# Kernel tuning notes

Hardware: AMD Instinct MI355X
Metric: run time of the kernel (lower is better)

The kernel has to match this reference:

```python
import jax, jax.numpy as jnp
import numpy as np

L, N, E, NODE_D, EDGE_D, H = 3, 50000, 800000, 64, 16, 128
EPS = 1e-5


def _ln(x, g, b):
    mu = jnp.mean(x, axis=-1, keepdims=True)
    var = jnp.var(x, axis=-1, keepdims=True)
    return (x - mu) * jax.lax.rsqrt(var + EPS) * g + b


def setup_inputs() -> dict:
    key = jax.random.key(0)
    ks = jax.random.split(key, 16)
    inp = {
        "x": jax.random.normal(ks[0], (N, NODE_D), dtype=jnp.float32),
        "edge_index": jax.random.randint(ks[1], (2, E), 0, N, dtype=jnp.int64 if jax.config.jax_enable_x64 else jnp.int32),
        "edge_attr": jax.random.normal(ks[2], (E, EDGE_D), dtype=jnp.float32),
        # node_embed: Linear(node_dim, H) + LayerNorm
        "node_W": jax.random.normal(ks[3], (H, NODE_D), dtype=jnp.float32) * (2.0 / H) ** 0.5,
        "node_b": jnp.zeros((H,), jnp.float32),
        "node_ln_g": jnp.ones((H,), jnp.float32),
        "node_ln_b": jnp.zeros((H,), jnp.float32),
        # per-layer GINConv params, stacked on leading layer dim
        "edge_W": jax.random.normal(ks[4], (L, H, EDGE_D), dtype=jnp.float32) * (2.0 / H) ** 0.5,
        "edge_b": jnp.zeros((L, H), jnp.float32),
        "edge_ln_g": jnp.ones((L, H), jnp.float32),
        "edge_ln_b": jnp.zeros((L, H), jnp.float32),
        "sl_attr": jax.random.normal(ks[5], (L, 1, EDGE_D), dtype=jnp.float32),
        "mlp_W1": jax.random.normal(ks[6], (L, 2 * H, H), dtype=jnp.float32) * (1.0 / H) ** 0.5,
        "mlp_b1": jnp.zeros((L, 2 * H), jnp.float32),
        "mlp_W2": jax.random.normal(ks[7], (L, H, 2 * H), dtype=jnp.float32) * (1.0 / (2 * H)) ** 0.5,
        "mlp_b2": jnp.zeros((L, H), jnp.float32),
        # BatchNorm1d affine params (batch-stat / training-mode math)
        "bn_g": jnp.ones((L, H), jnp.float32),
        "bn_b": jnp.zeros((L, H), jnp.float32),
    }
    return inp


def reference(x, edge_index, edge_attr, node_W, node_b, node_ln_g, node_ln_b,
              edge_W, edge_b, edge_ln_g, edge_ln_b, sl_attr,
              mlp_W1, mlp_b1, mlp_W2, mlp_b2, bn_g, bn_b):
    n = x.shape[0]
    # augmented edge list with self loops appended (add_self_loops)
    loop = jnp.arange(n, dtype=edge_index.dtype)
    src = jnp.concatenate([edge_index[0], loop])  # [E+N]
    dst = jnp.concatenate([edge_index[1], loop])  # [E+N]

    # node_embed: Linear -> LN -> ReLU
    h = jax.nn.relu(_ln(x @ node_W.T + node_b, node_ln_g, node_ln_b))

    for l in range(L):
        # edge_embed on [original edges ; learned self-loop attr]
        sl = jnp.broadcast_to(sl_attr[l], (n, EDGE_D))
        ea = jnp.concatenate([edge_attr, sl], axis=0)          # [E+N, edge_dim]
        ea = jax.nn.relu(_ln(ea @ edge_W[l].T + edge_b[l], edge_ln_g[l], edge_ln_b[l]))
        # message: gather x_j + edge_attr; aggregate: scatter-add to dst
        msg = h[src] + ea                                      # [E+N, H]
        aggr = jax.ops.segment_sum(msg, dst, num_segments=n)   # [N, H]
        # update MLP: Linear -> GELU -> Linear (dropout inactive at eval)
        z = jax.nn.gelu(aggr @ mlp_W1[l].T + mlp_b1[l], approximate=False)
        hl = z @ mlp_W2[l].T + mlp_b2[l]
        # BatchNorm1d (training-mode batch statistics over node dim)
        mu = jnp.mean(hl, axis=0, keepdims=True)
        var = jnp.var(hl, axis=0, keepdims=True)
        hl = (hl - mu) * jax.lax.rsqrt(var + EPS) * bn_g[l] + bn_b[l]
        if l != L - 1:
            hl = jax.nn.relu(hl)  # drop_ratio = 0 -> dropout is identity
        h = hl
    return h
```

## Files before the change

### kernel.cpp

```cpp
#include <hip/hip_runtime.h>
#include <cstdint>
#include <cstddef>

#define HD 128
#define EDGED 16
#define NODED 64
#define LN_EPS 1e-5f

typedef __bf16 bf16x8 __attribute__((ext_vector_type(8)));
typedef float  f32x4  __attribute__((ext_vector_type(4)));
typedef _Float16 half2v __attribute__((ext_vector_type(2)));
typedef _Float16 half4v __attribute__((ext_vector_type(4)));
typedef _Float16 half8v __attribute__((ext_vector_type(8)));

union HU { half8v v; half2v p[4]; };

__device__ __forceinline__ float gelu_exact(float x) {
    return 0.5f * x * (1.0f + erff(x * 0.7071067811865475f));
}

__device__ __forceinline__ float hi16_to_f(int bits) {
    union { unsigned short u; _Float16 h; } c;
    c.u = (unsigned short)((unsigned)bits >> 16);
    return (float)c.h;
}

__global__ void wconv_k(const float* __restrict__ in, __bf16* __restrict__ hi,
                        __bf16* __restrict__ lo, int n) {
    int i = blockIdx.x * blockDim.x + threadIdx.x;
    if (i < n) {
        float v = in[i];
        __bf16 h = (__bf16)v;
        hi[i] = h;
        lo[i] = (__bf16)(v - (float)h);
    }
}

__global__ void wconv16_k(const float* __restrict__ in, _Float16* __restrict__ hi,
                          _Float16* __restrict__ lo, int n) {
    int i = blockIdx.x * blockDim.x + threadIdx.x;
    if (i < n) {
        float v = in[i];
        _Float16 h = (_Float16)v;
        hi[i] = h;
        lo[i] = (_Float16)(v - (float)h);
    }
}


__global__ void hist_k(const int* __restrict__ ei, int* __restrict__ cnt, int E) {
    int e = blockIdx.x * blockDim.x + threadIdx.x;
    if (e < E) atomicAdd(&cnt[ei[E + e]], 1);
}

__global__ void scan1_k(const int* __restrict__ in, int* __restrict__ out,
                        int* __restrict__ bsum, int n) {
    __shared__ int lds[256];
    int t = threadIdx.x;
    int i = blockIdx.x * 256 + t;
    int v = (i < n) ? in[i] : 0;
    lds[t] = v;
    __syncthreads();
#pragma unroll
    for (int o = 1; o < 256; o <<= 1) {
        int u = (t >= o) ? lds[t - o] : 0;
        __syncthreads();
        lds[t] += u;
        __syncthreads();
    }
    if (i < n) out[i] = lds[t] - v;
    if (t == 255) bsum[blockIdx.x] = lds[255];
}

__global__ void scan2_k(const int* __restrict__ bsum, int* __restrict__ boff, int nb) {
    __shared__ int lds[256];
    int t = threadIdx.x;
    int v = (t < nb) ? bsum[t] : 0;
    lds[t] = v;
    __syncthreads();
#pragma unroll
    for (int o = 1; o < 256; o <<= 1) {
        int u = (t >= o) ? lds[t - o] : 0;
        __syncthreads();
        lds[t] += u;
        __syncthreads();
    }
    if (t < nb) boff[t] = lds[t] - v;
}

__global__ void scan3_k(int* __restrict__ rs, int* __restrict__ cursor,
                        const int* __restrict__ boff, int n, int E) {
    int i = blockIdx.x * 256 + threadIdx.x;
    if (i < n) {
        int v = rs[i] + boff[blockIdx.x];
        rs[i] = v;
        cursor[i] = v;
    }
    if (i == 0) rs[n] = E;
}

__global__ void scatter_k(const int* __restrict__ ei, int* __restrict__ cursor,
                          int2* __restrict__ es, int E) {
    int e = blockIdx.x * blockDim.x + threadIdx.x;
    if (e < E) {
        int dst = ei[E + e];
        int slot = atomicAdd(&cursor[dst], 1);
        es[slot] = make_int2(ei[e], e);
    }
}

__global__ void prep_k(const float* __restrict__ edge_W, const float* __restrict__ edge_b,
                       const float* __restrict__ edge_g, const float* __restrict__ edge_be,
                       const float* __restrict__ sl_attr, _Float16* __restrict__ Wg16_3,
                       float* __restrict__ bg3, float* __restrict__ M3,
                       float* __restrict__ v3, float* __restrict__ s03,
                       float* __restrict__ slv3)
{
    const int l = blockIdx.x;
    const float* W = edge_W + (size_t)l * HD * EDGED;
    const float* b = edge_b + l * HD;
    const float* g = edge_g + l * HD;
    __shared__ float Wp[HD * EDGED];
    __shared__ float bp[HD];
    __shared__ float wm[EDGED];
    __shared__ float Msh[256];
    __shared__ float vsh[EDGED];
    __shared__ float ash[EDGED];
    __shared__ float bmS, s0sh;
    const int t = threadIdx.x;
#pragma unroll
    for (int m = 0; m < 8; ++m) Wp[m * 256 + t] = W[m * 256 + t];
    __syncthreads();
    if (t < EDGED) {
        float s = 0.f;
        for (int c = 0; c < HD; ++c) s += Wp[c * EDGED + t];
        wm[t] = s * (1.f / HD);
    } else if (t == EDGED) {
        float s = 0.f;
        for (int c = 0; c < HD; ++c) s += b[c];
        bmS = s * (1.f / HD);
    }
    __syncthreads();
    if (t < HD) bp[t] = b[t] - bmS;
    __syncthreads();
#pragma unroll
    for (int m = 0; m < 8; ++m) {
        int idx = m * 256 + t;
        int c = idx >> 4, k = idx & 15;
        float val = Wp[idx] - wm[k];
        Wp[idx] = val;
        Wg16_3[(size_t)l * 2048 + idx] = (_Float16)(val * g[c]);
    }
    if (t < HD) bg3[l * HD + t] = bp[t] * g[t];
    __syncthreads();
    {
        int k = t >> 4, j = t & 15;
        float s = 0.f;
        for (int c = 0; c < HD; ++c) s += Wp[c * EDGED + k] * Wp[c * EDGED + j];
        Msh[t] = s;
        M3[l * 256 + t] = s;
    }
    if (t < EDGED) {
        float s = 0.f;
        for (int c = 0; c < HD; ++c) s += Wp[c * EDGED + t] * bp[c];
        vsh[t] = 2.f * s;
        v3[l * EDGED + t] = 2.f * s;
        ash[t] = sl_attr[l * EDGED + t];
    } else if (t == EDGED) {
        float s = 0.f;
        for (int c = 0; c < HD; ++c) s += bp[c] * bp[c];
        s0sh = s;
        s03[l] = s;
    }
    __syncthreads();
    if (t < HD) {
        float q = s0sh;
#pragma unroll
        for (int k = 0; k < EDGED; ++k) {
            float tk = vsh[k];
#pragma unroll
            for (int j = 0; j < EDGED; ++j) tk = fmaf(Msh[k * 16 + j], ash[j], tk);
            q = fmaf(ash[k], tk, q);
        }
        float inv = rsqrtf(q * (1.f / HD) + LN_EPS);
        float y = 0.f;
#pragma unroll
        for (int k = 0; k < EDGED; ++k) y = fmaf(Wp[t * EDGED + k], ash[k], y);
        slv3[l * HD + t] = fmaxf(fmaf(fmaf(y, g[t], bg3[l * HD + t]), inv, edge_be[l * HD + t]), 0.f);
    }
}

__launch_bounds__(256)
__global__ void einv_k(const int2* __restrict__ es, const float* __restrict__ eattr,
                       const float* __restrict__ M3, const float* __restrict__ v3,
                       const float* __restrict__ s03, unsigned* __restrict__ sei,
                       _Float16* __restrict__ attr16, int E)
{
    __shared__ float Ms[3 * 256];
    __shared__ float vs[3 * 16];
    __shared__ float s0s[4];
    const int t = threadIdx.x;
    for (int i = t; i < 768; i += 256) Ms[i] = M3[i];
    if (t < 48) vs[t] = v3[t];
    if (t < 3) s0s[t] = s03[t];
    __syncthreads();
    int slot = blockIdx.x * 256 + t;
    if (slot >= E) return;
    int2 se = es[slot];
    const float4* ap = (const float4*)(eattr + (size_t)se.y * EDGED);
    float4 A0 = ap[0], A1 = ap[1], A2 = ap[2], A3 = ap[3];
    float a[16] = {A0.x, A0.y, A0.z, A0.w, A1.x, A1.y, A1.z, A1.w,
                   A2.x, A2.y, A2.z, A2.w, A3.x, A3.y, A3.z, A3.w};
    {
        half8v o0, o1;
#pragma unroll
        for (int i = 0; i < 8; ++i) { o0[i] = (_Float16)a[i]; o1[i] = (_Float16)a[8 + i]; }
        _Float16* op = attr16 + (size_t)slot * EDGED;
        *(half8v*)&op[0] = o0;
        *(half8v*)&op[8] = o1;
    }
#pragma unroll
    for (int l = 0; l < 3; ++l) {
        float q = s0s[l];
#pragma unroll
        for (int k = 0; k < 16; ++k) {
            const float* Mr = &Ms[l * 256 + k * 16];
            float tk = vs[l * 16 + k];
#pragma unroll
            for (int j = 0; j < 16; ++j) tk = fmaf(Mr[j], a[j], tk);
            q = fmaf(a[k], tk, q);
        }
        float iv = rsqrtf(q * (1.f / HD) + LN_EPS);
        union { _Float16 h; unsigned short u; } cv;
        cv.h = (_Float16)iv;
        sei[(size_t)l * E + slot] = ((unsigned)se.x & 0xFFFFu) | ((unsigned)cv.u << 16);
    }
}

template<int K, int NC, int ACT, int STATS, int AMODE, int OUTMODE>
__launch_bounds__(256)
__global__ void mgemm_k(const void* __restrict__ Ap1, const void* __restrict__ Ap2,
                        const void* __restrict__ Wp1, const void* __restrict__ Wp2,
                        const float* __restrict__ bias, float* __restrict__ C,
                        void* __restrict__ Co1, int M, float* __restrict__ stats)
{
    constexpr int RG = 2;
    constexpr int NT = 4;
    constexpr int NK = K / 32;
    __shared__ float st_lds[2][64];

    const int t    = threadIdx.x;
    const int lane = t & 63;
    const int wv   = t >> 6;
    const int ln15 = lane & 15;
    const int quad = lane >> 4;
    const int row_base = blockIdx.x * 128 + wv * 32;
    const int col0 = blockIdx.y * 64;

    f32x4 acc[RG][NT];
#pragma unroll
    for (int g = 0; g < RG; ++g)
#pragma unroll
        for (int nt = 0; nt < NT; ++nt)
#pragma unroll
            for (int r = 0; r < 4; ++r) acc[g][nt][r] = 0.f;

    size_t arow[RG];
#pragma unroll
    for (int g = 0; g < RG; ++g) {
        int row = row_base + g * 16 + ln15;
        row = row < M ? row : M - 1;
        arow[g] = (size_t)row * K + quad * 8;
    }
    size_t brow[NT];
#pragma unroll
    for (int nt = 0; nt < NT; ++nt)
        brow[nt] = (size_t)(col0 + nt * 16 + ln15) * K + quad * 8;

    if constexpr (AMODE == 0) {
        const __bf16* Ahi = (const __bf16*)Ap1;
        const __bf16* Alo = (const __bf16*)Ap2;
        const __bf16* Whi = (const __bf16*)Wp1;
        const __bf16* Wlo = (const __bf16*)Wp2;
        bf16x8 a0h[RG], a0l[RG], a1h[RG], a1l[RG];
        bf16x8 b0h[NT], b0l[NT], b1h[NT], b1l[NT];

#define LD_A(kc, AH, AL) { \
    _Pragma("unroll") \
    for (int g = 0; g < RG; ++g) { \
        AH[g] = *(const bf16x8*)(Ahi + arow[g] + (kc)); \
        AL[g] = *(const bf16x8*)(Alo + arow[g] + (kc)); \
    } }
#define LD_B(kc, BH, BL) { \
    _Pragma("unroll") \
    for (int nt = 0; nt < NT; ++nt) { \
        BH[nt] = *(const bf16x8*)(Whi + brow[nt] + (kc)); \
        BL[nt] = *(const bf16x8*)(Wlo + brow[nt] + (kc)); \
    } }
#define DO_MFMA(AH, AL, BH, BL) { \
    _Pragma("unroll") \
    for (int nt = 0; nt < NT; ++nt) { \
        _Pragma("unroll") \
        for (int g = 0; g < RG; ++g) { \
            acc[g][nt] = __builtin_amdgcn_mfma_f32_16x16x32_bf16(AH[g], BH[nt], acc[g][nt], 0, 0, 0); \
            acc[g][nt] = __builtin_amdgcn_mfma_f32_16x16x32_bf16(AH[g], BL[nt], acc[g][nt], 0, 0, 0); \
            acc[g][nt] = __builtin_amdgcn_mfma_f32_16x16x32_bf16(AL[g], BH[nt], acc[g][nt], 0, 0, 0); \
        } } }

        LD_A(0, a0h, a0l);
        LD_B(0, b0h, b0l);
        for (int s = 0; s < NK; s += 2) {
            LD_A((s + 1) * 32, a1h, a1l);
            LD_B((s + 1) * 32, b1h, b1l);
            DO_MFMA(a0h, a0l, b0h, b0l);
            if (s + 2 < NK) {
                LD_A((s + 2) * 32, a0h, a0l);
                LD_B((s + 2) * 32, b0h, b0l);
            }
            DO_MFMA(a1h, a1l, b1h, b1l);
        }
#undef LD_A
#undef LD_B
#undef DO_MFMA
    } else {
        const _Float16* Af = (const _Float16*)Ap1;
        const _Float16* Wh = (const _Float16*)Wp1;
        const _Float16* Wl = (const _Float16*)Wp2;
        half8v a0[RG], a1[RG];
        half8v b0h[NT], b0l[NT], b1h[NT], b1l[NT];

#define LD_A16(kc, A) { \
    _Pragma("unroll") \
    for (int g = 0; g < RG; ++g) A[g] = *(const half8v*)(Af + arow[g] + (kc)); }
#define LD_B16(kc, BH, BL) { \
    _Pragma("unroll") \
    for (int nt = 0; nt < NT; ++nt) { \
        BH[nt] = *(const half8v*)(Wh + brow[nt] + (kc)); \
        BL[nt] = *(const half8v*)(Wl + brow[nt] + (kc)); \
    } }
#define DO_MFMA16(A, BH, BL) { \
    _Pragma("unroll") \
    for (int nt = 0; nt < NT; ++nt) { \
        _Pragma("unroll") \
        for (int g = 0; g < RG; ++g) { \
            acc[g][nt] = __builtin_amdgcn_mfma_f32_16x16x32_f16(A[g], BH[nt], acc[g][nt], 0, 0, 0); \
            acc[g][nt] = __builtin_amdgcn_mfma_f32_16x16x32_f16(A[g], BL[nt], acc[g][nt], 0, 0, 0); \
        } } }

        LD_A16(0, a0);
        LD_B16(0, b0h, b0l);
        for (int s = 0; s < NK; s += 2) {
            LD_A16((s + 1) * 32, a1);
            LD_B16((s + 1) * 32, b1h, b1l);
            DO_MFMA16(a0, b0h, b0l);
            if (s + 2 < NK) {
                LD_A16((s + 2) * 32, a0);
                LD_B16((s + 2) * 32, b0h, b0l);
            }
            DO_MFMA16(a1, b1h, b1l);
        }
#undef LD_A16
#undef LD_B16
#undef DO_MFMA16
    }

    if (STATS) {
        if (t < 64) { st_lds[0][t] = 0.f; st_lds[1][t] = 0.f; }
        __syncthreads();
    }

    float bv[NT];
#pragma unroll
    for (int nt = 0; nt < NT; ++nt) bv[nt] = bias[col0 + nt * 16 + ln15];

    float s1[NT], s2[NT];
#pragma unroll
    for (int nt = 0; nt < NT; ++nt) { s1[nt] = 0.f; s2[nt] = 0.f; }

#pragma unroll
    for (int g = 0; g < RG; ++g)
#pragma unroll
        for (int r = 0; r < 4; ++r) {
            int row = row_base + g * 16 + quad * 4 + r;
            if (row < M) {
#pragma unroll
                for (int nt = 0; nt < NT; ++nt) {
                    float v = acc[g][nt][r] + bv[nt];
                    if (ACT == 1) v = gelu_exact(v);
                    size_t ci = (size_t)row * NC + col0 + nt * 16 + ln15;
                    if (OUTMODE == 2) {
                        ((_Float16*)Co1)[ci] = (_Float16)v;
                    } else {
                        C[ci] = v;
                    }
                    if (STATS) { s1[nt] += v; s2[nt] += v * v; }
                }
            }
        }

    if (STATS) {
#pragma unroll
        for (int nt = 0; nt < NT; ++nt) {
            atomicAdd(&st_lds[0][nt * 16 + ln15], s1[nt]);
            atomicAdd(&st_lds[1][nt * 16 + ln15], s2[nt]);
        }
        __syncthreads();
        if (t < 64) {
            atomicAdd(&stats[col0 + t],      st_lds[0][t]);
            atomicAdd(&stats[HD + col0 + t], st_lds[1][t]);
        }
    }
}

__launch_bounds__(256)
__global__ void nemb_k(const __bf16* __restrict__ Ahi, const __bf16* __restrict__ Alo,
                       const __bf16* __restrict__ Whi, const __bf16* __restrict__ Wlo,
                       const float* __restrict__ bias, const float* __restrict__ gam,
                       const float* __restrict__ bet, _Float16* __restrict__ h16, int M)
{
    constexpr int RG = 2;
    constexpr int NT = 8;
    const int t    = threadIdx.x;
    const int lane = t & 63;
    const int wv   = t >> 6;
    const int ln15 = lane & 15;
    const int quad = lane >> 4;
    const int row_base = blockIdx.x * 128 + wv * 32;

    f32x4 acc[RG][NT];
#pragma unroll
    for (int g = 0; g < RG; ++g)
#pragma unroll
        for (int nt = 0; nt < NT; ++nt)
#pragma unroll
            for (int r = 0; r < 4; ++r) acc[g][nt][r] = 0.f;

    size_t arow[RG];
#pragma unroll
    for (int g = 0; g < RG; ++g) {
        int row = row_base + g * 16 + ln15;
        row = row < M ? row : M - 1;
        arow[g] = (size_t)row * NODED + quad * 8;
    }
    size_t brow[NT];
#pragma unroll
    for (int nt = 0; nt < NT; ++nt)
        brow[nt] = (size_t)(nt * 16 + ln15) * NODED + quad * 8;

#pragma unroll
    for (int s = 0; s < 2; ++s) {
        bf16x8 ah[RG], al[RG];
#pragma unroll
        for (int g = 0; g < RG; ++g) {
            ah[g] = *(const bf16x8*)(Ahi + arow[g] + s * 32);
            al[g] = *(const bf16x8*)(Alo + arow[g] + s * 32);
        }
#pragma unroll
        for (int nt = 0; nt < NT; ++nt) {
            bf16x8 bh = *(const bf16x8*)(Whi + brow[nt] + s * 32);
            bf16x8 bl = *(const bf16x8*)(Wlo + brow[nt] + s * 32);
#pragma unroll
            for (int g = 0; g < RG; ++g) {
                acc[g][nt] = __builtin_amdgcn_mfma_f32_16x16x32_bf16(ah[g], bh, acc[g][nt], 0, 0, 0);
                acc[g][nt] = __builtin_amdgcn_mfma_f32_16x16x32_bf16(ah[g], bl, acc[g][nt], 0, 0, 0);
                acc[g][nt] = __builtin_amdgcn_mfma_f32_16x16x32_bf16(al[g], bh, acc[g][nt], 0, 0, 0);
            }
        }
    }

    float bv[NT], gv[NT], betv[NT];
#pragma unroll
    for (int nt = 0; nt < NT; ++nt) {
        int col = nt * 16 + ln15;
        bv[nt]   = bias[col];
        gv[nt]   = gam[col];
        betv[nt] = bet[col];
    }

#pragma unroll
    for (int g = 0; g < RG; ++g)
#pragma unroll
        for (int r = 0; r < 4; ++r) {
            int row = row_base + g * 16 + quad * 4 + r;
            float v[NT];
            float s = 0.f, q = 0.f;
#pragma unroll
            for (int nt = 0; nt < NT; ++nt) {
                v[nt] = acc[g][nt][r] + bv[nt];
                s += v[nt];
                q += v[nt] * v[nt];
            }
#pragma unroll
            for (int o = 8; o > 0; o >>= 1) {
                s += __shfl_xor(s, o, 64);
                q += __shfl_xor(q, o, 64);
            }
            float mu  = s * (1.f / 128.f);
            float inv = rsqrtf(q * (1.f / 128.f) - mu * mu + LN_EPS);
            if (row < M) {
#pragma unroll
                for (int nt = 0; nt < NT; ++nt) {
                    float rr = fmaxf(fmaf((v[nt] - mu) * inv, gv[nt], betv[nt]), 0.f);
                    h16[(size_t)row * HD + nt * 16 + ln15] = (_Float16)rr;
                }
            }
        }
}

__launch_bounds__(256)
__global__ void pull9_k(const _Float16* __restrict__ h16, const int* __restrict__ rs,
                        const _Float16* __restrict__ attr16, const unsigned* __restrict__ sei,
                        const float* __restrict__ slv, const _Float16* __restrict__ Wg16,
                        const float* __restrict__ bg, const float* __restrict__ bet,
                        __bf16* __restrict__ Ahi, __bf16* __restrict__ Alo, int N)
{
    __shared__ _Float16 alds_all[4][64 * EDGED];
    const int t = threadIdx.x;
    const int lane = t & 63;
    const int wv = t >> 6;
    _Float16* alds = alds_all[wv];
    uint4* alds4 = (uint4*)alds;

    const int c0 = lane * 2;
    half2v w0p[8], w1p[8];
#pragma unroll
    for (int k = 0; k < 8; ++k) {
        w0p[k] = *(const half2v*)&Wg16[c0 * EDGED + 2 * k];
        w1p[k] = *(const half2v*)&Wg16[(c0 + 1) * EDGED + 2 * k];
    }
    const float2 bgv  = *(const float2*)&bg[c0];
    const float2 btv  = *(const float2*)&bet[c0];
    const float2 slvv = *(const float2*)&slv[c0];

    const int stride = gridDim.x << 2;
    for (int n = (blockIdx.x << 2) + wv; n < N; n += stride) {
        half2v hs = *(const half2v*)&h16[(size_t)n * HD + c0];
        float acc0 = (float)hs.x + slvv.x;
        float acc1 = (float)hs.y + slvv.y;

        const int beg = rs[n], end = rs[n + 1];
        for (int s0 = beg; s0 < end; s0 += 64) {
            int m = end - s0; if (m > 64) m = 64;
            int sv = 0;
            if (lane < m) sv = (int)sei[s0 + lane];
            const uint4* src4 = (const uint4*)(attr16 + (size_t)s0 * EDGED);
#pragma unroll
            for (int it = 0; it < 2; ++it) {
                int idx = (it << 6) + lane;
                if (idx < (m << 1)) alds4[idx] = src4[idx];
            }
            asm volatile("s_waitcnt lgkmcnt(0)" ::: "memory");

#define EDGE_BODY(JJ, IVJ, HVJ) { \
            HU ua, ub; \
            ua.v = *(const half8v*)&alds[(JJ) * EDGED]; \
            ub.v = *(const half8v*)&alds[(JJ) * EDGED + 8]; \
            float p0 = bgv.x, q0 = 0.f, p1 = bgv.y, q1 = 0.f; \
            p0 = __builtin_amdgcn_fdot2(ua.p[0], w0p[0], p0, false); \
            q0 = __builtin_amdgcn_fdot2(ua.p[1], w0p[1], q0, false); \
            p1 = __builtin_amdgcn_fdot2(ua.p[0], w1p[0], p1, false); \
            q1 = __builtin_amdgcn_fdot2(ua.p[1], w1p[1], q1, false); \
            p0 = __builtin_amdgcn_fdot2(ua.p[2], w0p[2], p0, false); \
            q0 = __builtin_amdgcn_fdot2(ua.p[3], w0p[3], q0, false); \
            p1 = __builtin_amdgcn_fdot2(ua.p[2], w1p[2], p1, false); \
            q1 = __builtin_amdgcn_fdot2(ua.p[3], w1p[3], q1, false); \
            p0 = __builtin_amdgcn_fdot2(ub.p[0], w0p[4], p0, false); \
            q0 = __builtin_amdgcn_fdot2(ub.p[1], w0p[5], q0, false); \
            p1 = __builtin_amdgcn_fdot2(ub.p[0], w1p[4], p1, false); \
            q1 = __builtin_amdgcn_fdot2(ub.p[1], w1p[5], q1, false); \
            p0 = __builtin_amdgcn_fdot2(ub.p[2], w0p[6], p0, false); \
            q0 = __builtin_amdgcn_fdot2(ub.p[3], w0p[7], q0, false); \
            p1 = __builtin_amdgcn_fdot2(ub.p[2], w1p[6], p1, false); \
            q1 = __builtin_amdgcn_fdot2(ub.p[3], w1p[7], q1, false); \
            acc0 += fmaxf(fmaf(p0 + q0, IVJ, btv.x), 0.f) + (float)HVJ.x; \
            acc1 += fmaxf(fmaf(p1 + q1, IVJ, btv.y), 0.f) + (float)HVJ.y; \
        }

            int j = 0;
            for (; j + 4 <= m; j += 4) {
                int v0 = __shfl(sv, j,     64);
                int v1 = __shfl(sv, j + 1, 64);
                int v2 = __shfl(sv, j + 2, 64);
                int v3 = __shfl(sv, j + 3, 64);
                int s_0 = v0 & 0xFFFF, s_1 = v1 & 0xFFFF;
                int s_2 = v2 & 0xFFFF, s_3 = v3 & 0xFFFF;
                float i0 = hi16_to_f(v0);
                float i1 = hi16_to_f(v1);
                float i2 = hi16_to_f(v2);
                float i3 = hi16_to_f(v3);
                half2v h0 = *(const half2v*)&h16[(size_t)s_0 * HD + c0];
                half2v h1 = *(const half2v*)&h16[(size_t)s_1 * HD + c0];
                half2v h2 = *(const half2v*)&h16[(size_t)s_2 * HD + c0];
                half2v h3 = *(const half2v*)&h16[(size_t)s_3 * HD + c0];
                EDGE_BODY(j,     i0, h0);
                EDGE_BODY(j + 1, i1, h1);
                EDGE_BODY(j + 2, i2, h2);
                EDGE_BODY(j + 3, i3, h3);
            }
            for (; j < m; ++j) {
                int vj = __shfl(sv, j, 64);
                int s_ = vj & 0xFFFF;
                float ij = hi16_to_f(vj);
                half2v hj = *(const half2v*)&h16[(size_t)s_ * HD + c0];
                EDGE_BODY(j, ij, hj);
            }
#undef EDGE_BODY
        }
        __bf16 b0 = (__bf16)acc0, b1 = (__bf16)acc1;
        union { __bf16 b[2]; unsigned u; } ph, pl;
        ph.b[0] = b0;
        ph.b[1] = b1;
        pl.b[0] = (__bf16)(acc0 - (float)b0);
        pl.b[1] = (__bf16)(acc1 - (float)b1);
        *(unsigned*)&Ahi[(size_t)n * HD + c0] = ph.u;
        *(unsigned*)&Alo[(size_t)n * HD + c0] = pl.u;
    }
}

__global__ void bn_k(const _Float16* __restrict__ hl, const float* __restrict__ stats,
                     const float* __restrict__ gam, const float* __restrict__ bet,
                     float* __restrict__ out32, _Float16* __restrict__ out16,
                     int total4, float invN, int relu)
{
    int idx = blockIdx.x * blockDim.x + threadIdx.x;
    if (idx < total4) {
        int c4 = idx & 31;
        half4v xh = *(const half4v*)&hl[(size_t)idx * 4];
        float4 s1 = ((const float4*)stats)[c4];
        float4 s2 = ((const float4*)stats)[32 + c4];
        float4 g  = ((const float4*)gam)[c4];
        float4 b  = ((const float4*)bet)[c4];
        float4 r;
        {
            float m = s1.x * invN; float v = s2.x * invN - m * m;
            r.x = fmaf(((float)xh.x - m) * rsqrtf(v + LN_EPS), g.x, b.x);
        }
        {
            float m = s1.y * invN; float v = s2.y * invN - m * m;
            r.y = fmaf(((float)xh.y - m) * rsqrtf(v + LN_EPS), g.y, b.y);
        }
        {
            float m = s1.z * invN; float v = s2.z * invN - m * m;
            r.z = fmaf(((float)xh.z - m) * rsqrtf(v + LN_EPS), g.z, b.z);
        }
        {
            float m = s1.w * invN; float v = s2.w * invN - m * m;
            r.w = fmaf(((float)xh.w - m) * rsqrtf(v + LN_EPS), g.w, b.w);
        }
        if (relu) {
            r.x = fmaxf(r.x, 0.f); r.y = fmaxf(r.y, 0.f);
            r.z = fmaxf(r.z, 0.f); r.w = fmaxf(r.w, 0.f);
        }
        if (out16) {
            half4v o;
            o.x = (_Float16)r.x; o.y = (_Float16)r.y;
            o.z = (_Float16)r.z; o.w = (_Float16)r.w;
            *(half4v*)&out16[(size_t)idx * 4] = o;
        } else {
            ((float4*)out32)[idx] = r;
        }
    }
}

extern "C" void kernel_launch(void* const* d_in, const int* in_sizes, int n_in,
                              void* d_out, int out_size, void* d_ws, size_t ws_size,
                              hipStream_t stream)
{
    const float* x       = (const float*)d_in[0];
    const int*   ei      = (const int*)d_in[1];
    const float* eattr   = (const float*)d_in[2];
    const float* node_W  = (const float*)d_in[3];
    const float* node_b  = (const float*)d_in[4];
    const float* node_g  = (const float*)d_in[5];
    const float* node_be = (const float*)d_in[6];
    const float* edge_W  = (const float*)d_in[7];
    const float* edge_b  = (const float*)d_in[8];
    const float* edge_g  = (const float*)d_in[9];
    const float* edge_be = (const float*)d_in[10];
    const float* sl_attr = (const float*)d_in[11];
    const float* W1      = (const float*)d_in[12];
    const float* b1      = (const float*)d_in[13];
    const float* W2      = (const float*)d_in[14];
    const float* b2      = (const float*)d_in[15];
    const float* bn_g    = (const float*)d_in[16];
    const float* bn_b    = (const float*)d_in[17];

    const int N = in_sizes[0] / NODED;
    const int E = in_sizes[1] / 2;

    char* base = (char*)d_ws;
    size_t off = 0;
    auto take = [&](size_t nbytes) -> void* {
        void* p = base + off;
        off = (off + nbytes + 15) & ~(size_t)15;
        return p;
    };
    _Float16* h16  = (_Float16*)take((size_t)N * HD * 2);
    _Float16* hl16 = (_Float16*)take((size_t)N * HD * 2);
    __bf16* aghi   = (__bf16*)take((size_t)N * HD * 2);
    __bf16* aglo   = (__bf16*)take((size_t)N * HD * 2);
    _Float16* z16  = (_Float16*)take((size_t)N * 256 * 2);
    __bf16* xhi    = (__bf16*)take((size_t)N * NODED * 2);
    __bf16* xlo    = (__bf16*)take((size_t)N * NODED * 2);
    float*  slv3   = (float*)take(3 * HD * 4);
    float*  stats  = (float*)take(3 * 256 * 4);
    int*    cnt    = (int*)take((size_t)N * 4);
    int*    cursor = (int*)take((size_t)N * 4);
    int*    bsum   = (int*)take(256 * 4);
    int*    boff   = (int*)take(256 * 4);
    int*    rs     = (int*)take(((size_t)N + 2) * 4);
    int2*   es     = (int2*)take((size_t)E * 8);
    unsigned* sei  = (unsigned*)take((size_t)3 * E * 4);
    _Float16* attr16 = (_Float16*)take((size_t)E * EDGED * 2);
    _Float16* Wg16_3 = (_Float16*)take(3 * 2048 * 2);
    float*  bg3    = (float*)take(3 * HD * 4);
    float*  M3     = (float*)take(3 * 256 * 4);
    float*  v3     = (float*)take(3 * 16 * 4);
    float*  s03    = (float*)take(4 * 4);
    __bf16* nWhi   = (__bf16*)take((size_t)HD * NODED * 2);
    __bf16* nWlo   = (__bf16*)take((size_t)HD * NODED * 2);
    __bf16* W1hi   = (__bf16*)take((size_t)3 * 256 * HD * 2);
    __bf16* W1lo   = (__bf16*)take((size_t)3 * 256 * HD * 2);
    _Float16* W2h16 = (_Float16*)take((size_t)3 * HD * 256 * 2);
    _Float16* W2l16 = (_Float16*)take((size_t)3 * HD * 256 * 2);

    wconv_k<<<(HD * NODED + 255) / 256, 256, 0, stream>>>(node_W, nWhi, nWlo, HD * NODED);
    wconv_k<<<(3 * 256 * HD + 255) / 256, 256, 0, stream>>>(W1, W1hi, W1lo, 3 * 256 * HD);
    wconv16_k<<<(3 * 256 * HD + 255) / 256, 256, 0, stream>>>(W2, W2h16, W2l16, 3 * 256 * HD);
    wconv_k<<<((int)((size_t)N * NODED + 255) / 256), 256, 0, stream>>>(x, xhi, xlo, N * NODED);

    prep_k<<<3, 256, 0, stream>>>(edge_W, edge_b, edge_g, edge_be, sl_attr,
                                  Wg16_3, bg3, M3, v3, s03, slv3);

    const int eblocks = (E + 255) / 256;
    const int nblocks = (N + 255) / 256;
    hipMemsetAsync(cnt, 0, (size_t)N * sizeof(int), stream);
    hist_k<<<eblocks, 256, 0, stream>>>(ei, cnt, E);
    scan1_k<<<nblocks, 256, 0, stream>>>(cnt, rs, bsum, N);
    scan2_k<<<1, 256, 0, stream>>>(bsum, boff, nblocks);
    scan3_k<<<nblocks, 256, 0, stream>>>(rs, cursor, boff, N, E);
    scatter_k<<<eblocks, 256, 0, stream>>>(ei, cursor, es, E);

    einv_k<<<eblocks, 256, 0, stream>>>(es, eattr, M3, v3, s03, sei, attr16, E);

    const int total4  = N * (HD / 4);
    const int vblocks = (total4 + 255) / 256;
    const int gb128   = (N + 127) / 128;
    int pgrid = (N + 3) / 4;
    if (pgrid > 2048) pgrid = 2048;

    nemb_k<<<gb128, 256, 0, stream>>>(xhi, xlo, nWhi, nWlo, node_b,
                                      node_g, node_be, h16, N);

    hipMemsetAsync(stats, 0, 3 * 256 * sizeof(float), stream);

    for (int l = 0; l < 3; ++l) {
        pull9_k<<<pgrid, 256, 0, stream>>>(h16, rs, attr16, sei + (size_t)l * E,
                                           slv3 + l * HD, Wg16_3 + (size_t)l * 2048,
                                           bg3 + l * HD, edge_be + l * HD,
                                           aghi, aglo, N);

        mgemm_k<HD, 256, 1, 0, 0, 2><<<dim3(gb128, 4), 256, 0, stream>>>(
            aghi, aglo, W1hi + (size_t)l * 256 * HD, W1lo + (size_t)l * 256 * HD,
            b1 + l * 256, nullptr, z16, N, nullptr);

        mgemm_k<256, HD, 0, 1, 1, 2><<<dim3(gb128, 2), 256, 0, stream>>>(
            z16, nullptr, W2h16 + (size_t)l * HD * 256, W2l16 + (size_t)l * HD * 256,
            b2 + l * HD, nullptr, hl16, N, stats + l * 256);

        bn_k<<<vblocks, 256, 0, stream>>>(hl16, stats + l * 256,
                                          bn_g + l * HD, bn_b + l * HD,
                                          (float*)d_out, (l < 2) ? h16 : nullptr,
                                          total4, 1.f / N, (l < 2) ? 1 : 0);
    }
}
```

Measured before the change: 871.7 us.

## Fuse the two MLP GEMMs into one kernel keeping GELU activations in LDS

Replaces the two separate MLP GEMM launches with a single kernel. Each wave computes its 32x256 GELU intermediate into shared memory, then runs the second GEMM from LDS and accumulates the BatchNorm statistics. This removes the global write and re-read of the N x 256 half-precision intermediate and one launch per layer. In exchange it uses 64KB of LDS per block, which limits occupancy, and the software double-buffering of the first GEMM's loads is dropped.

```diff
diff --git a/kernel.cpp b/kernel.cpp
--- a/kernel.cpp
+++ b/kernel.cpp
@@ -237,17 +237,17 @@
     }
 }
 
-template<int K, int NC, int ACT, int STATS, int AMODE, int OUTMODE>
 __launch_bounds__(256)
-__global__ void mgemm_k(const void* __restrict__ Ap1, const void* __restrict__ Ap2,
-                        const void* __restrict__ Wp1, const void* __restrict__ Wp2,
-                        const float* __restrict__ bias, float* __restrict__ C,
-                        void* __restrict__ Co1, int M, float* __restrict__ stats)
+__global__ void fmlp_k(const __bf16* __restrict__ Ahi, const __bf16* __restrict__ Alo,
+                       const __bf16* __restrict__ W1hi, const __bf16* __restrict__ W1lo,
+                       const float* __restrict__ b1, const _Float16* __restrict__ W2h,
+                       const _Float16* __restrict__ W2l, const float* __restrict__ b2,
+                       _Float16* __restrict__ hl16, int M, float* __restrict__ stats)
 {
     constexpr int RG = 2;
-    constexpr int NT = 4;
-    constexpr int NK = K / 32;
-    __shared__ float st_lds[2][64];
+    constexpr int NT = 8;
+    __shared__ _Float16 zlds_all[4][32 * 256];
+    __shared__ float st_lds[2][128];
 
     const int t    = threadIdx.x;
     const int lane = t & 63;
@@ -255,127 +255,99 @@
     const int ln15 = lane & 15;
     const int quad = lane >> 4;
     const int row_base = blockIdx.x * 128 + wv * 32;
-    const int col0 = blockIdx.y * 64;
-
-    f32x4 acc[RG][NT];
-#pragma unroll
-    for (int g = 0; g < RG; ++g)
-#pragma unroll
-        for (int nt = 0; nt < NT; ++nt)
-#pragma unroll
-            for (int r = 0; r < 4; ++r) acc[g][nt][r] = 0.f;
+    _Float16* zl = zlds_all[wv];
 
     size_t arow[RG];
 #pragma unroll
     for (int g = 0; g < RG; ++g) {
         int row = row_base + g * 16 + ln15;
         row = row < M ? row : M - 1;
-        arow[g] = (size_t)row * K + quad * 8;
-    }
-    size_t brow[NT];
-#pragma unroll
-    for (int nt = 0; nt < NT; ++nt)
-        brow[nt] = (size_t)(col0 + nt * 16 + ln15) * K + quad * 8;
-
-    if constexpr (AMODE == 0) {
-        const __bf16* Ahi = (const __bf16*)Ap1;
-        const __bf16* Alo = (const __bf16*)Ap2;
-        const __bf16* Whi = (const __bf16*)Wp1;
-        const __bf16* Wlo = (const __bf16*)Wp2;
-        bf16x8 a0h[RG], a0l[RG], a1h[RG], a1l[RG];
-        bf16x8 b0h[NT], b0l[NT], b1h[NT], b1l[NT];
-
-#define LD_A(kc, AH, AL) { \
-    _Pragma("unroll") \
-    for (int g = 0; g < RG; ++g) { \
-        AH[g] = *(const bf16x8*)(Ahi + arow[g] + (kc)); \
-        AL[g] = *(const bf16x8*)(Alo + arow[g] + (kc)); \
-    } }
-#define LD_B(kc, BH, BL) { \
-    _Pragma("unroll") \
-    for (int nt = 0; nt < NT; ++nt) { \
-        BH[nt] = *(const bf16x8*)(Whi + brow[nt] + (kc)); \
-        BL[nt] = *(const bf16x8*)(Wlo + brow[nt] + (kc)); \
-    } }
-#define DO_MFMA(AH, AL, BH, BL) { \
-    _Pragma("unroll") \
-    for (int nt = 0; nt < NT; ++nt) { \
-        _Pragma("unroll") \
-        for (int g = 0; g < RG; ++g) { \
-            acc[g][nt] = __builtin_amdgcn_mfma_f32_16x16x32_bf16(AH[g], BH[nt], acc[g][nt], 0, 0, 0); \
-            acc[g][nt] = __builtin_amdgcn_mfma_f32_16x16x32_bf16(AH[g], BL[nt], acc[g][nt], 0, 0, 0); \
-            acc[g][nt] = __builtin_amdgcn_mfma_f32_16x16x32_bf16(AL[g], BH[nt], acc[g][nt], 0, 0, 0); \
-        } } }
-
-        LD_A(0, a0h, a0l);
-        LD_B(0, b0h, b0l);
-        for (int s = 0; s < NK; s += 2) {
-            LD_A((s + 1) * 32, a1h, a1l);
-            LD_B((s + 1) * 32, b1h, b1l);
-            DO_MFMA(a0h, a0l, b0h, b0l);
-            if (s + 2 < NK) {
-                LD_A((s + 2) * 32, a0h, a0l);
-                LD_B((s + 2) * 32, b0h, b0l);
-            }
-            DO_MFMA(a1h, a1l, b1h, b1l);
-        }
-#undef LD_A
-#undef LD_B
-#undef DO_MFMA
-    } else {
-        const _Float16* Af = (const _Float16*)Ap1;
-        const _Float16* Wh = (const _Float16*)Wp1;
-        const _Float16* Wl = (const _Float16*)Wp2;
-        half8v a0[RG], a1[RG];
-        half8v b0h[NT], b0l[NT], b1h[NT], b1l[NT];
-
-#define LD_A16(kc, A) { \
-    _Pragma("unroll") \
-    for (int g = 0; g < RG; ++g) A[g] = *(const half8v*)(Af + arow[g] + (kc)); }
-#define LD_B16(kc, BH, BL) { \
-    _Pragma("unroll") \
-    for (int nt = 0; nt < NT; ++nt) { \
-        BH[nt] = *(const half8v*)(Wh + brow[nt] + (kc)); \
-        BL[nt] = *(const half8v*)(Wl + brow[nt] + (kc)); \
-    } }
-#define DO_MFMA16(A, BH, BL) { \
-    _Pragma("unroll") \
-    for (int nt = 0; nt < NT; ++nt) { \
-        _Pragma("unroll") \
-        for (int g = 0; g < RG; ++g) { \
-            acc[g][nt] = __builtin_amdgcn_mfma_f32_16x16x32_f16(A[g], BH[nt], acc[g][nt], 0, 0, 0); \
-            acc[g][nt] = __builtin_amdgcn_mfma_f32_16x16x32_f16(A[g], BL[nt], acc[g][nt], 0, 0, 0); \
-        } } }
-
-        LD_A16(0, a0);
-        LD_B16(0, b0h, b0l);
-        for (int s = 0; s < NK; s += 2) {
-            LD_A16((s + 1) * 32, a1);
-            LD_B16((s + 1) * 32, b1h, b1l);
-            DO_MFMA16(a0, b0h, b0l);
-            if (s + 2 < NK) {
-                LD_A16((s + 2) * 32, a0);
-                LD_B16((s + 2) * 32, b0h, b0l);
-            }
-            DO_MFMA16(a1, b1h, b1l);
-        }
-#undef LD_A16
-#undef LD_B16
-#undef DO_MFMA16
-    }
-
-    if (STATS) {
-        if (t < 64) { st_lds[0][t] = 0.f; st_lds[1][t] = 0.f; }
-        __syncthreads();
-    }
-
-    float bv[NT];
-#pragma unroll
-    for (int nt = 0; nt < NT; ++nt) bv[nt] = bias[col0 + nt * 16 + ln15];
-
-    float s1[NT], s2[NT];
-#pragma unroll
-    for (int nt = 0; nt < NT; ++nt) { s1[nt] = 0.f; s2[nt] = 0.f; }
+        arow[g] = (size_t)row * HD + quad * 8;
+    }
+
+#pragma unroll
+    for (int h = 0; h < 2; ++h) {
+        const int col0 = h * 128;
+        f32x4 acc[RG][NT];
+#pragma unroll
+        for (int g = 0; g < RG; ++g)
+#pragma unroll
+            for (int nt = 0; nt < NT; ++nt)
+#pragma unroll
+                for (int r = 0; r < 4; ++r) acc[g][nt][r] = 0.f;
+
+#pragma unroll
+        for (int s = 0; s < 4; ++s) {
+            bf16x8 ah[RG], al[RG];
+#pragma unroll
+            for (int g = 0; g < RG; ++g) {
+                ah[g] = *(const bf16x8*)(Ahi + arow[g] + s * 32);
+                al[g] = *(const bf16x8*)(Alo + arow[g] + s * 32);
+            }
+#pragma unroll
+            for (int nt = 0; nt < NT; ++nt) {
+                size_t br = (size_t)(col0 + nt * 16 + ln15) * HD + quad * 8 + s * 32;
+                bf16x8 bh = *(const bf16x8*)(W1hi + br);
+                bf16x8 bl = *(const bf16x8*)(W1lo + br);
+#pragma unroll
+                for (int g = 0; g < RG; ++g) {
+                    acc[g][nt] = __builtin_amdgcn_mfma_f32_16x16x32_bf16(ah[g], bh, acc[g][nt], 0, 0, 0);
+                    acc[g][nt] = __builtin_amdgcn_mfma_f32_16x16x32_bf16(ah[g], bl, acc[g][nt], 0, 0, 0);
+                    acc[g][nt] = __builtin_amdgcn_mfma_f32_16x16x32_bf16(al[g], bh, acc[g][nt], 0, 0, 0);
+                }
+            }
+        }
+
+#pragma unroll
+        for (int g = 0; g < RG; ++g)
+#pragma unroll
+            for (int r = 0; r < 4; ++r) {
+                int lr = g * 16 + quad * 4 + r;
+#pragma unroll
+                for (int nt = 0; nt < NT; ++nt) {
+                    int col = col0 + nt * 16 + ln15;
+                    float v = gelu_exact(acc[g][nt][r] + b1[col]);
+                    zl[lr * 256 + col] = (_Float16)v;
+                }
+            }
+    }
+
+    if (t < 128) { st_lds[0][t] = 0.f; st_lds[1][t] = 0.f; }
+    __syncthreads();
+
+    f32x4 acc2[RG][NT];
+#pragma unroll
+    for (int g = 0; g < RG; ++g)
+#pragma unroll
+        for (int nt = 0; nt < NT; ++nt)
+#pragma unroll
+            for (int r = 0; r < 4; ++r) acc2[g][nt][r] = 0.f;
+
+#pragma unroll
+    for (int s = 0; s < 8; ++s) {
+        half8v az[RG];
+#pragma unroll
+        for (int g = 0; g < RG; ++g)
+            az[g] = *(const half8v*)&zl[(g * 16 + ln15) * 256 + s * 32 + quad * 8];
+#pragma unroll
+        for (int nt = 0; nt < NT; ++nt) {
+            size_t br = (size_t)(nt * 16 + ln15) * 256 + quad * 8 + s * 32;
+            half8v wh = *(const half8v*)(W2h + br);
+            half8v wl = *(const half8v*)(W2l + br);
+#pragma unroll
+            for (int g = 0; g < RG; ++g) {
+                acc2[g][nt] = __builtin_amdgcn_mfma_f32_16x16x32_f16(az[g], wh, acc2[g][nt], 0, 0, 0);
+                acc2[g][nt] = __builtin_amdgcn_mfma_f32_16x16x32_f16(az[g], wl, acc2[g][nt], 0, 0, 0);
+            }
+        }
+    }
+
+    float bv[NT], s1[NT], s2[NT];
+#pragma unroll
+    for (int nt = 0; nt < NT; ++nt) {
+        bv[nt] = b2[nt * 16 + ln15];
+        s1[nt] = 0.f; s2[nt] = 0.f;
+    }
 
 #pragma unroll
     for (int g = 0; g < RG; ++g)
@@ -385,30 +357,23 @@
             if (row < M) {
 #pragma unroll
                 for (int nt = 0; nt < NT; ++nt) {
-                    float v = acc[g][nt][r] + bv[nt];
-                    if (ACT == 1) v = gelu_exact(v);
-                    size_t ci = (size_t)row * NC + col0 + nt * 16 + ln15;
-                    if (OUTMODE == 2) {
-                        ((_Float16*)Co1)[ci] = (_Float16)v;
-                    } else {
-                        C[ci] = v;
-                    }
-                    if (STATS) { s1[nt] += v; s2[nt] += v * v; }
+                    float v = acc2[g][nt][r] + bv[nt];
+                    hl16[(size_t)row * HD + nt * 16 + ln15] = (_Float16)v;
+                    s1[nt] += v;
+                    s2[nt] += v * v;
                 }
             }
         }
 
-    if (STATS) {
-#pragma unroll
-        for (int nt = 0; nt < NT; ++nt) {
-            atomicAdd(&st_lds[0][nt * 16 + ln15], s1[nt]);
-            atomicAdd(&st_lds[1][nt * 16 + ln15], s2[nt]);
-        }
-        __syncthreads();
-        if (t < 64) {
-            atomicAdd(&stats[col0 + t],      st_lds[0][t]);
-            atomicAdd(&stats[HD + col0 + t], st_lds[1][t]);
-        }
+#pragma unroll
+    for (int nt = 0; nt < NT; ++nt) {
+        atomicAdd(&st_lds[0][nt * 16 + ln15], s1[nt]);
+        atomicAdd(&st_lds[1][nt * 16 + ln15], s2[nt]);
+    }
+    __syncthreads();
+    if (t < 128) {
+        atomicAdd(&stats[t],      st_lds[0][t]);
+        atomicAdd(&stats[HD + t], st_lds[1][t]);
     }
 }
 
@@ -699,7 +664,6 @@
     _Float16* hl16 = (_Float16*)take((size_t)N * HD * 2);
     __bf16* aghi   = (__bf16*)take((size_t)N * HD * 2);
     __bf16* aglo   = (__bf16*)take((size_t)N * HD * 2);
-    _Float16* z16  = (_Float16*)take((size_t)N * 256 * 2);
     __bf16* xhi    = (__bf16*)take((size_t)N * NODED * 2);
     __bf16* xlo    = (__bf16*)take((size_t)N * NODED * 2);
     float*  slv3   = (float*)take(3 * HD * 4);
@@ -760,13 +724,10 @@
                                            bg3 + l * HD, edge_be + l * HD,
                                            aghi, aglo, N);
 
-        mgemm_k<HD, 256, 1, 0, 0, 2><<<dim3(gb128, 4), 256, 0, stream>>>(
+        fmlp_k<<<gb128, 256, 0, stream>>>(
             aghi, aglo, W1hi + (size_t)l * 256 * HD, W1lo + (size_t)l * 256 * HD,
-            b1 + l * 256, nullptr, z16, N, nullptr);
-
-        mgemm_k<256, HD, 0, 1, 1, 2><<<dim3(gb128, 2), 256, 0, stream>>>(
-            z16, nullptr, W2h16 + (size_t)l * HD * 256, W2l16 + (size_t)l * HD * 256,
-            b2 + l * HD, nullptr, hl16, N, stats + l * 256);
+            b1 + l * 256, W2h16 + (size_t)l * HD * 256, W2l16 + (size_t)l * HD * 256,
+            b2 + l * HD, hl16, N, stats + l * 256);
 
         bn_k<<<vblocks, 256, 0, stream>>>(hl16, stats + l * 256,
                                           bn_g + l * HD, bn_b + l * HD,
```

Measured after the change: 832.0 us. 4.5% less time.
